# Optimization experiments

Hardware: AMD Instinct MI355X
Metric: run time of the kernel (lower is better)

The kernel has to match this reference:

```python
import jax, jax.numpy as jnp
import numpy as np

N = 6890          # SMPL vertex count
C = 1024          # number of presented-contact vertices
CONTACT_THRESH = 1.0  # contact_thresh default


def setup_inputs() -> dict:
    key = jax.random.key(0)
    k1, k2, k3 = jax.random.split(key, 3)
    vertices = jax.random.normal(k1, (1, N, 3), dtype=jnp.float32)
    presented_contact = jax.random.randint(k2, (C,), 0, N)
    geomask = jax.random.randint(k3, (N, N), 0, 2).astype(bool)
    return {"presented_contact": presented_contact, "vertices": vertices, "geomask": geomask}


def reference(presented_contact, vertices, geomask):
    verts = vertices[0]  # [N, 3]  (batch squeeze)
    # Full pairwise Euclidean distance matrix, as in the torch module
    diff = verts[:, None, :] - verts[None, :, :]        # [N, N, 3]
    v2v = jnp.linalg.norm(diff, ord=2, axis=-1)          # [N, N]

    # Restrict to contact vertices
    c = v2v[presented_contact][:, presented_contact]     # [C, C]
    mg = geomask[presented_contact][:, presented_contact]  # [C, C] bool

    # (dist + 1) weighted by 1 where geodesically allowed, inf otherwise
    scores = jnp.where(mg, c + 1.0, jnp.inf)             # [C, C]
    min_idx = presented_contact[jnp.argmin(scores, axis=1)]  # [C] absolute vertex ids
    min_idx = jax.lax.stop_gradient(min_idx)             # computed under no_grad in torch

    v2v_min = v2v[presented_contact, min_idx]            # [C]
    # contact_mode == 'dist_tanh'
    contactloss = (CONTACT_THRESH * jnp.tanh(v2v_min / CONTACT_THRESH)).mean()
    return contactloss
```

## Files before the change

kernel.cpp:

```cpp
#include <hip/hip_runtime.h>
#include <hip/hip_bf16.h>
#include <math.h>

#define NV 6890
#define NC 1024

__global__ void detect_mode_kernel(const unsigned int* __restrict__ gm,
                                   int* __restrict__ flag) {
    if (threadIdx.x == 0 && blockIdx.x == 0) {
        int byteMode = 0;
        for (int k = 0; k < 64; ++k) {
            unsigned int w = gm[k];
            if (!(w == 0u || w == 1u || w == 0x3F800000u)) { byteMode = 1; break; }
        }
        flag[0] = byteMode;
    }
}

__global__ __launch_bounds__(256) void contact_row_kernel(
        const int* __restrict__ pc, const float* __restrict__ verts,
        const void* __restrict__ gm, const int* __restrict__ flag,
        float* __restrict__ tvals, float* __restrict__ atom_out, int atomicMode) {
    __shared__ float sx[NC], sy[NC], sz[NC];
    __shared__ int   spc[NC];
    __shared__ float wbest[4];
    __shared__ int   widx[4];

    const int tid = threadIdx.x;
    for (int j = tid; j < NC; j += 256) {
        int v = pc[j];
        spc[j] = v;
        sx[j] = verts[3 * v + 0];
        sy[j] = verts[3 * v + 1];
        sz[j] = verts[3 * v + 2];
    }
    __syncthreads();

    const int   i  = blockIdx.x;
    const float xi = sx[i], yi = sy[i], zi = sz[i];
    const int   vi = spc[i];
    const int   byteMode = flag[0];
    const unsigned char* gmb = (const unsigned char*)gm + (size_t)vi * NV;
    const unsigned int*  gmi = (const unsigned int*)gm  + (size_t)vi * NV;

    float best = INFINITY;
    int   bidx = 0x7FFFFFFF;
    for (int j = tid; j < NC; j += 256) {
        float dx = xi - sx[j], dy = yi - sy[j], dz = zi - sz[j];
        float d2 = dx * dx + dy * dy + dz * dz;
        int vj = spc[j];
        unsigned int m = byteMode ? (unsigned int)gmb[vj] : gmi[vj];
        float s = m ? d2 : INFINITY;
        if (s < best || (s == best && j < bidx)) { best = s; bidx = j; }
    }

    #pragma unroll
    for (int off = 32; off > 0; off >>= 1) {
        float ob = __shfl_down(best, off, 64);
        int   oi = __shfl_down(bidx, off, 64);
        if (ob < best || (ob == best && oi < bidx)) { best = ob; bidx = oi; }
    }
    if ((tid & 63) == 0) { wbest[tid >> 6] = best; widx[tid >> 6] = bidx; }
    __syncthreads();

    if (tid == 0) {
        best = wbest[0]; bidx = widx[0];
        #pragma unroll
        for (int w = 1; w < 4; ++w) {
            if (wbest[w] < best || (wbest[w] == best && widx[w] < bidx)) {
                best = wbest[w]; bidx = widx[w];
            }
        }
        float dx = xi - sx[bidx], dy = yi - sy[bidx], dz = zi - sz[bidx];
        float d  = sqrtf(dx * dx + dy * dy + dz * dz);
        float t  = tanhf(d);
        if (atomicMode) {
            atomicAdd(atom_out, t * (1.0f / (float)NC));
        } else {
            tvals[i] = t;
        }
    }
}

__global__ __launch_bounds__(256) void reduce_mean_kernel(
        const float* __restrict__ vals, float* __restrict__ out) {
    __shared__ float wsum[4];
    const int t = threadIdx.x;
    float s = vals[t] + vals[t + 256] + vals[t + 512] + vals[t + 768];
    #pragma unroll
    for (int off = 32; off > 0; off >>= 1) s += __shfl_down(s, off, 64);
    if ((t & 63) == 0) wsum[t >> 6] = s;
    __syncthreads();
    if (t == 0) out[0] = (wsum[0] + wsum[1] + wsum[2] + wsum[3]) * (1.0f / (float)NC);
}

extern "C" void kernel_launch(void* const* d_in, const int* in_sizes, int n_in,
                              void* d_out, int out_size, void* d_ws, size_t ws_size,
                              hipStream_t stream) {
    const int*   pc    = (const int*)d_in[0];
    const float* verts = (const float*)d_in[1];
    const void*  gm    = d_in[2];
    float*       out   = (float*)d_out;

    int* flag = (int*)d_ws;

    detect_mode_kernel<<<1, 64, 0, stream>>>((const unsigned int*)gm, flag);

    if (ws_size >= 256 + NC * sizeof(float)) {
        float* tvals = (float*)((char*)d_ws + 256);
        contact_row_kernel<<<NC, 256, 0, stream>>>(pc, verts, gm, flag, tvals, nullptr, 0);
        reduce_mean_kernel<<<1, 256, 0, stream>>>(tvals, out);
    } else {
        hipMemsetAsync(d_out, 0, sizeof(float), stream);
        contact_row_kernel<<<NC, 256, 0, stream>>>(pc, verts, gm, flag, nullptr, out, 1);
    }
}
```

Measured before the change: 243.5 us.

## Stage full geomask row in shared memory and fold mode detection into main kernel

Each block now loads its entire geomask row coalesced into a shared byte array, then does the masked argmin with shared-memory lookups instead of scattered global gathers. The separate mode-detection kernel is replaced by an in-block ballot over the first 64 words, and the atomic fallback path is dropped. The aim is to replace latency-bound random gathers with streaming reads and to cut a launch. In exchange it reads more bytes per row and uses more shared memory, which lowers occupancy. It also assumes the workspace is large enough.

```diff
diff --git a/kernel.cpp b/kernel.cpp
--- a/kernel.cpp
+++ b/kernel.cpp
@@ -5,28 +5,25 @@
 #define NV 6890
 #define NC 1024
 
-__global__ void detect_mode_kernel(const unsigned int* __restrict__ gm,
-                                   int* __restrict__ flag) {
-    if (threadIdx.x == 0 && blockIdx.x == 0) {
-        int byteMode = 0;
-        for (int k = 0; k < 64; ++k) {
-            unsigned int w = gm[k];
-            if (!(w == 0u || w == 1u || w == 0x3F800000u)) { byteMode = 1; break; }
-        }
-        flag[0] = byteMode;
-    }
-}
-
 __global__ __launch_bounds__(256) void contact_row_kernel(
         const int* __restrict__ pc, const float* __restrict__ verts,
-        const void* __restrict__ gm, const int* __restrict__ flag,
-        float* __restrict__ tvals, float* __restrict__ atom_out, int atomicMode) {
+        const void* __restrict__ gm, float* __restrict__ tvals) {
     __shared__ float sx[NC], sy[NC], sz[NC];
     __shared__ int   spc[NC];
+    __shared__ unsigned char rowm[NV];
+    __shared__ int   modeSh;
     __shared__ float wbest[4];
     __shared__ int   widx[4];
 
     const int tid = threadIdx.x;
+
+    if (tid < 64) {
+        unsigned int w = ((const unsigned int*)gm)[tid];
+        bool ok4 = (w == 0u || w == 1u || w == 0x3F800000u);
+        unsigned long long b = __ballot(ok4);
+        if (tid == 0) modeSh = (b == ~0ULL) ? 0 : 1;
+    }
+
     for (int j = tid; j < NC; j += 256) {
         int v = pc[j];
         spc[j] = v;
@@ -36,21 +33,28 @@
     }
     __syncthreads();
 
-    const int   i  = blockIdx.x;
+    const int i  = blockIdx.x;
+    const int vi = spc[i];
+    const int mode = modeSh;
+
+    if (mode == 0) {
+        const unsigned int* row = (const unsigned int*)gm + (size_t)vi * NV;
+        for (int k = tid; k < NV; k += 256) rowm[k] = (unsigned char)(row[k] != 0u);
+    } else {
+        const unsigned char* row = (const unsigned char*)gm + (size_t)vi * NV;
+        for (int k = tid; k < NV; k += 256) rowm[k] = row[k];
+    }
+    __syncthreads();
+
     const float xi = sx[i], yi = sy[i], zi = sz[i];
-    const int   vi = spc[i];
-    const int   byteMode = flag[0];
-    const unsigned char* gmb = (const unsigned char*)gm + (size_t)vi * NV;
-    const unsigned int*  gmi = (const unsigned int*)gm  + (size_t)vi * NV;
-
     float best = INFINITY;
     int   bidx = 0x7FFFFFFF;
-    for (int j = tid; j < NC; j += 256) {
+    #pragma unroll
+    for (int u = 0; u < NC / 256; ++u) {
+        int j = tid + u * 256;
         float dx = xi - sx[j], dy = yi - sy[j], dz = zi - sz[j];
         float d2 = dx * dx + dy * dy + dz * dz;
-        int vj = spc[j];
-        unsigned int m = byteMode ? (unsigned int)gmb[vj] : gmi[vj];
-        float s = m ? d2 : INFINITY;
+        float s = rowm[spc[j]] ? d2 : INFINITY;
         if (s < best || (s == best && j < bidx)) { best = s; bidx = j; }
     }
 
@@ -73,12 +77,7 @@
         }
         float dx = xi - sx[bidx], dy = yi - sy[bidx], dz = zi - sz[bidx];
         float d  = sqrtf(dx * dx + dy * dy + dz * dz);
-        float t  = tanhf(d);
-        if (atomicMode) {
-            atomicAdd(atom_out, t * (1.0f / (float)NC));
-        } else {
-            tvals[i] = t;
-        }
+        tvals[i] = tanhf(d);
     }
 }
 
@@ -102,16 +101,8 @@
     const void*  gm    = d_in[2];
     float*       out   = (float*)d_out;
 
-    int* flag = (int*)d_ws;
+    float* tvals = (float*)d_ws;
 
-    detect_mode_kernel<<<1, 64, 0, stream>>>((const unsigned int*)gm, flag);
-
-    if (ws_size >= 256 + NC * sizeof(float)) {
-        float* tvals = (float*)((char*)d_ws + 256);
-        contact_row_kernel<<<NC, 256, 0, stream>>>(pc, verts, gm, flag, tvals, nullptr, 0);
-        reduce_mean_kernel<<<1, 256, 0, stream>>>(tvals, out);
-    } else {
-        hipMemsetAsync(d_out, 0, sizeof(float), stream);
-        contact_row_kernel<<<NC, 256, 0, stream>>>(pc, verts, gm, flag, nullptr, out, 1);
-    }
+    contact_row_kernel<<<NC, 256, 0, stream>>>(pc, verts, gm, tvals);
+    reduce_mean_kernel<<<1, 256, 0, stream>>>(tvals, out);
 }
```

Result: faster. 235.0 us (-3.5%).
